# Kernel optimization log

Measured on AMD Instinct MI355X. Metric: run time of the kernel, lower is better.

Reference implementation:

```python
import jax, jax.numpy as jnp
import numpy as np

B, S, H = 2, 1024, 2048
HEADS = 16
QC = 1536      # q_compressed_dim
KVC = 512      # kv_compressed_dim
ROPE = 64      # qk_rope_dim
NOPE = H // HEADS  # 128, non-rope head dim
VH = 128       # v_head_dim
INTER = 1408   # MoE intermediate dim
NSH = 2        # shared experts
NRT = 8        # routed experts
TOPK = 2
EPS = 1e-6


def setup_inputs() -> dict:
    key = jax.random.key(0)
    ks = jax.random.split(key, 16)

    def w(k, shape, scale=0.02):
        return jax.random.normal(k, shape, jnp.float32) * scale

    return {
        "x": jax.random.normal(ks[0], (B, S, H), jnp.float32),
        "freq": jax.random.uniform(ks[1], (S, ROPE // 2), jnp.float32, 0.0, 2.0 * np.pi),
        "mask": jnp.zeros((S, S), jnp.float32),
        "w_attn_norm": jnp.ones((H,), jnp.float32),
        "w_ffn_norm": jnp.ones((H,), jnp.float32),
        "W_dq": w(ks[2], (H, QC)),
        "q_c_norm": jnp.ones((QC,), jnp.float32),
        "W_uq": w(ks[3], (QC, HEADS * (NOPE + ROPE))),
        "W_dkv": w(ks[4], (H, KVC + ROPE)),
        "kv_c_norm": jnp.ones((KVC,), jnp.float32),
        "W_ukv": w(ks[5], (KVC, HEADS * (NOPE + VH))),
        "W_o": w(ks[6], (HEADS * VH, H)),
        "W_r": w(ks[7], (H, NRT)),
        "Ws_gate": w(ks[8], (NSH, H, INTER)),
        "Ws_up": w(ks[9], (NSH, H, INTER)),
        "Ws_down": w(ks[10], (NSH, INTER, H)),
        "We_gate": w(ks[11], (NRT, H, INTER)),
        "We_up": w(ks[12], (NRT, H, INTER)),
        "We_down": w(ks[13], (NRT, INTER, H)),
    }


def rmsnorm(x, w):
    return x * jax.lax.rsqrt(jnp.mean(x * x, axis=-1, keepdims=True) + EPS) * w


def rope_apply(x, cos, sin):
    # x: [..., S, D]; cos/sin: [S, D/2], interleaved-pair rotation
    x1 = x[..., 0::2]
    x2 = x[..., 1::2]
    return jnp.stack([x1 * cos - x2 * sin, x1 * sin + x2 * cos], axis=-1).reshape(x.shape)


def _experts(t, Wg, Wu, Wd):
    # t: [T,H]; W*: [E,H,I]/[E,I,H] -> [E,T,H], SwiGLU per expert
    hid = jax.nn.silu(jnp.einsum('th,ehi->eti', t, Wg)) * jnp.einsum('th,ehi->eti', t, Wu)
    return jnp.einsum('eti,eih->eth', hid, Wd)


def reference(x, freq, mask, w_attn_norm, w_ffn_norm, W_dq, q_c_norm, W_uq, W_dkv,
              kv_c_norm, W_ukv, W_o, W_r, Ws_gate, Ws_up, Ws_down,
              We_gate, We_up, We_down):
    Bb, Ss, Hh = x.shape
    cos = jnp.cos(freq)
    sin = jnp.sin(freq)

    # ---- MLA attention (pre-norm) ----
    h = rmsnorm(x, w_attn_norm)
    cq = rmsnorm(h @ W_dq, q_c_norm)                              # [B,S,QC]
    q = (cq @ W_uq).reshape(Bb, Ss, HEADS, NOPE + ROPE).transpose(0, 2, 1, 3)
    q_nope, q_rope = q[..., :NOPE], q[..., NOPE:]
    q_rope = rope_apply(q_rope, cos, sin)                          # [B,Hh,S,ROPE]

    ckv = h @ W_dkv                                               # [B,S,KVC+ROPE]
    kv_c = rmsnorm(ckv[..., :KVC], kv_c_norm)
    k_rope = rope_apply(ckv[..., KVC:], cos, sin)                  # [B,S,ROPE] shared over heads
    kv = (kv_c @ W_ukv).reshape(Bb, Ss, HEADS, NOPE + VH).transpose(0, 2, 1, 3)
    k_nope, v = kv[..., :NOPE], kv[..., NOPE:]

    scale = 1.0 / np.sqrt(NOPE + ROPE)
    scores = (jnp.einsum('bhsd,bhtd->bhst', q_nope, k_nope)
              + jnp.einsum('bhsd,btd->bhst', q_rope, k_rope)) * scale + mask
    attn = jax.nn.softmax(scores, axis=-1)
    attn_out = jnp.einsum('bhst,bhtd->bshd', attn, v).reshape(Bb, Ss, HEADS * VH) @ W_o
    x = x + attn_out

    # ---- DeepSeekMoE FFN (pre-norm) ----
    t = rmsnorm(x, w_ffn_norm).reshape(Bb * Ss, Hh)
    shared = _experts(t, Ws_gate, Ws_up, Ws_down).sum(axis=0)      # [T,H]
    probs = jax.nn.softmax(t @ W_r, axis=-1)                       # [T,E]
    vals, idx = jax.lax.top_k(probs, TOPK)
    weights = (jax.nn.one_hot(idx, NRT, dtype=t.dtype) * vals[..., None]).sum(axis=1)  # [T,E]
    routed = jnp.einsum('eth,te->th', _experts(t, We_gate, We_up, We_down), weights)
    return x + (shared + routed).reshape(Bb, Ss, Hh)
```

## Files before the change

kernel.cpp:

```cpp
#include <hip/hip_runtime.h>

typedef __bf16 bf16;
typedef _Float16 f16;
typedef unsigned short u16;
typedef __bf16 bf16x8 __attribute__((ext_vector_type(8)));
typedef _Float16 f16x8 __attribute__((ext_vector_type(8)));
typedef unsigned short u16x8 __attribute__((ext_vector_type(8)));
typedef float f32x4 __attribute__((ext_vector_type(4)));

#define TOK   2048
#define SEQ   1024
#define HIDD  2048
#define NHEADS 16
#define QCD   1536
#define KVCD  512
#define ROPED 64
#define NOPED 128
#define QDIM  192
#define VHD   128
#define KVD   576
#define KVDP  640
#define INTERD 1408
#define GUD   2816
#define RMS_EPS 1e-6f
#define SPS   64.0f
#define OSC   (1.0f/4096.0f)

__device__ inline void split64(float v, f16& h, f16& l) {
    v *= SPS; h = (f16)v; l = (f16)(v - (float)h);
}

__device__ inline void gl_lds16(const void* g, void* l) {
    __builtin_amdgcn_global_load_lds(
        (const __attribute__((address_space(1))) void*)g,
        (__attribute__((address_space(3))) void*)l,
        16, 0, 0);
}

__global__ __launch_bounds__(256) void tconv_kernel(const float* __restrict__ src,
                                                    bf16* __restrict__ dst,
                                                    int K, int N, int Npad) {
    __shared__ float tile[32][33];
    int nb = blockIdx.x * 32, kb = blockIdx.y * 32;
    int tx = threadIdx.x & 31, ty = threadIdx.x >> 5;
#pragma unroll
    for (int i = 0; i < 32; i += 8) {
        int k = kb + ty + i, n = nb + tx;
        tile[ty + i][tx] = (k < K && n < N) ? src[(long)k * N + n] : 0.f;
    }
    __syncthreads();
#pragma unroll
    for (int i = 0; i < 32; i += 8) {
        int n = nb + ty + i, k = kb + tx;
        if (n < Npad && k < K) dst[(long)n * K + k] = (bf16)tile[tx][ty + i];
    }
}

__global__ __launch_bounds__(256) void tconv3h_kernel(const float* __restrict__ src,
                                                      f16* __restrict__ dst,
                                                      int K, int N, int Npad) {
    __shared__ float tile[32][33];
    int nb = blockIdx.x * 32, kb = blockIdx.y * 32;
    int tx = threadIdx.x & 31, ty = threadIdx.x >> 5;
#pragma unroll
    for (int i = 0; i < 32; i += 8) {
        int k = kb + ty + i, n = nb + tx;
        tile[ty + i][tx] = (k < K && n < N) ? src[(long)k * N + n] : 0.f;
    }
    __syncthreads();
#pragma unroll
    for (int i = 0; i < 32; i += 8) {
        int n = nb + ty + i, k = kb + tx;
        if (n < Npad && k < K) {
            f16 h, l; split64(tile[tx][ty + i], h, l);
            long base = (long)n * (3 * K) + k;
            dst[base] = h; dst[base + K] = l; dst[base + 2 * K] = h;
        }
    }
}

template<int F16, int TM, int TN>
__global__ __launch_bounds__(256) void gemm_bt_kernel(
    const u16* __restrict__ A, const u16* __restrict__ B, void* __restrict__ Cv,
    const float* __restrict__ aux, const int* __restrict__ idx,
    const int* __restrict__ cntPtr,
    int K, int lda, int ldb, int ldc,
    long sA, long sB, long sC,
    int mode, int auxLd, float osc)
{
    constexpr int AM = TM / 32;
    constexpr int AN = TN / 32;
    __shared__ u16 As[2][TM * 64];
    __shared__ u16 Bs[2][TN * 64];
    const int bn = blockIdx.x, bm = blockIdx.y, z = blockIdx.z;
    int cnt = 1 << 30;
    if (cntPtr) {
        cnt = *cntPtr;
        int pad = (cnt + TM - 1) & ~(TM - 1);
        if (bm * TM >= pad) return;
    }
    const int tid = threadIdx.x, lane = tid & 63, w = tid >> 6;
    const int wm = w >> 1, wn = w & 1;
    const int lr = lane & 15;
    const int srow = lane >> 3, c16 = lane & 7;
    const u16* Ab = A + (long)z * sA + (long)bm * TM * lda;
    const u16* Bb = B + (long)z * sB + (long)bn * TN * ldb;
    f32x4 acc[AM][AN] = {};

    auto stage = [&](int buf, int k0) {
#pragma unroll
        for (int i = 0; i < TM / 32; i++) {
            int rb = i * 32 + w * 8;
            int row = rb + srow;
            int gc = ((c16 ^ (row & 7)) << 3);
            gl_lds16(&Ab[(long)row * lda + k0 + gc], &As[buf][rb * 64]);
        }
#pragma unroll
        for (int i = 0; i < TN / 32; i++) {
            int rb = i * 32 + w * 8;
            int row = rb + srow;
            int gc = ((c16 ^ (row & 7)) << 3);
            gl_lds16(&Bb[(long)row * ldb + k0 + gc], &Bs[buf][rb * 64]);
        }
    };

    const int nk = K >> 6;
    stage(0, 0);
    __syncthreads();
    for (int t = 0; t < nk; ++t) {
        const int cur = t & 1;
        if (t + 1 < nk) stage(cur ^ 1, (t + 1) << 6);
#pragma unroll
        for (int ks = 0; ks < 2; ks++) {
            u16x8 af[AM], bfr[AN];
#pragma unroll
            for (int mi = 0; mi < AM; mi++) {
                int row = wm * (TM / 2) + mi * 16 + lr;
                int cg = (ks * 4 + (lane >> 4)) ^ (row & 7);
                af[mi] = *(const u16x8*)&As[cur][row * 64 + cg * 8];
            }
#pragma unroll
            for (int ni = 0; ni < AN; ni++) {
                int row = wn * (TN / 2) + ni * 16 + lr;
                int cg = (ks * 4 + (lane >> 4)) ^ (row & 7);
                bfr[ni] = *(const u16x8*)&Bs[cur][row * 64 + cg * 8];
            }
#pragma unroll
            for (int mi = 0; mi < AM; mi++)
#pragma unroll
                for (int ni = 0; ni < AN; ni++) {
                    if constexpr (F16)
                        acc[mi][ni] = __builtin_amdgcn_mfma_f32_16x16x32_f16(
                            __builtin_bit_cast(f16x8, af[mi]),
                            __builtin_bit_cast(f16x8, bfr[ni]), acc[mi][ni], 0, 0, 0);
                    else
                        acc[mi][ni] = __builtin_amdgcn_mfma_f32_16x16x32_bf16(
                            __builtin_bit_cast(bf16x8, af[mi]),
                            __builtin_bit_cast(bf16x8, bfr[ni]), acc[mi][ni], 0, 0, 0);
                }
        }
        __syncthreads();
    }

    const int r0 = (lane >> 4) << 2;
    const int rowBase = bm * TM + wm * (TM / 2);
    const int colBase = bn * TN + wn * (TN / 2);
#pragma unroll
    for (int mi = 0; mi < AM; mi++) {
#pragma unroll
        for (int ni = 0; ni < AN; ni++) {
#pragma unroll
            for (int r = 0; r < 4; r++) {
                int row = rowBase + mi * 16 + r0 + r;
                int col = colBase + ni * 16 + lr;
                float val = acc[mi][ni][r] * osc;
                long ci = (long)z * sC + (long)row * ldc + col;
                if (mode == 0) {
                    ((float*)Cv)[ci] = val;
                } else if (mode == 2) {
                    ((float*)Cv)[ci] = val + aux[(long)row * auxLd + col];
                } else if (mode == 3) {
                    float s = aux ? aux[(long)row * auxLd] : 1.f;
                    ((float*)Cv)[ci] += s * val;
                } else if (mode == 5) {
                    if (row < cnt) {
                        int tok = idx[row];
                        ((float*)Cv)[(long)tok * ldc + col] += aux[(long)tok * auxLd] * val;
                    }
                } else {
                    f16 h = (f16)val; f16 l = (f16)(val - (float)h);
                    ((f16*)Cv)[ci] = h; ((f16*)Cv)[ci + auxLd] = h; ((f16*)Cv)[ci + 2 * auxLd] = l;
                }
            }
        }
    }
}

__global__ __launch_bounds__(256) void rmsnorm_kernel(const float* __restrict__ in,
                                                      const float* __restrict__ w,
                                                      bf16* __restrict__ outB,
                                                      float* __restrict__ copyOut, int C) {
    long row = blockIdx.x;
    const float* r = in + row * C;
    float ss = 0.f;
    for (int i = threadIdx.x; i < C; i += 256) { float v = r[i]; ss += v * v; }
    for (int off = 32; off > 0; off >>= 1) ss += __shfl_down(ss, off, 64);
    __shared__ float red[5];
    int lane = threadIdx.x & 63, wv = threadIdx.x >> 6;
    if (lane == 0) red[wv] = ss;
    __syncthreads();
    if (threadIdx.x == 0) red[4] = rsqrtf((red[0] + red[1] + red[2] + red[3]) / C + RMS_EPS);
    __syncthreads();
    float sc = red[4];
    for (int i = threadIdx.x; i < C; i += 256) {
        outB[row * C + i] = (bf16)(r[i] * sc * w[i]);
        if (copyOut) copyOut[row * C + i] = r[i];
    }
}

__global__ __launch_bounds__(256) void rmsnorm3h_kernel(const float* __restrict__ in,
                                                        const float* __restrict__ w,
                                                        f16* __restrict__ out3, int C) {
    long row = blockIdx.x;
    const float* r = in + row * C;
    float ss = 0.f;
    for (int i = threadIdx.x; i < C; i += 256) { float v = r[i]; ss += v * v; }
    for (int off = 32; off > 0; off >>= 1) ss += __shfl_down(ss, off, 64);
    __shared__ float red[5];
    int lane = threadIdx.x & 63, wv = threadIdx.x >> 6;
    if (lane == 0) red[wv] = ss;
    __syncthreads();
    if (threadIdx.x == 0) red[4] = rsqrtf((red[0] + red[1] + red[2] + red[3]) / C + RMS_EPS);
    __syncthreads();
    float sc = red[4];
    f16* o = out3 + row * (3L * C);
    for (int i = threadIdx.x; i < C; i += 256) {
        f16 h, l; split64(r[i] * sc * w[i], h, l);
        o[i] = h; o[C + i] = h; o[2 * C + i] = l;
    }
}

__global__ __launch_bounds__(256) void kvsplit3h_kernel(const float* __restrict__ ckv,
                                                        const float* __restrict__ nrm,
                                                        const float* __restrict__ freq,
                                                        f16* __restrict__ kvc3,
                                                        float* __restrict__ krope) {
    int t = blockIdx.x; int s = t & (SEQ - 1);
    const float* r = ckv + (long)t * KVDP;
    float ss = 0.f;
    for (int i = threadIdx.x; i < KVCD; i += 256) { float v = r[i]; ss += v * v; }
    for (int off = 32; off > 0; off >>= 1) ss += __shfl_down(ss, off, 64);
    __shared__ float red[5];
    int lane = threadIdx.x & 63, wv = threadIdx.x >> 6;
    if (lane == 0) red[wv] = ss;
    __syncthreads();
    if (threadIdx.x == 0) red[4] = rsqrtf((red[0] + red[1] + red[2] + red[3]) / KVCD + RMS_EPS);
    __syncthreads();
    float sc = red[4];
    f16* o = kvc3 + (long)t * (3 * KVCD);
    for (int i = threadIdx.x; i < KVCD; i += 256) {
        f16 h, l; split64(r[i] * sc * nrm[i], h, l);
        o[i] = h; o[KVCD + i] = h; o[2 * KVCD + i] = l;
    }
    if (threadIdx.x < 32) {
        int i = threadIdx.x;
        float f = freq[s * 32 + i], c = cosf(f), sn = sinf(f);
        float x1 = r[KVCD + 2 * i], x2 = r[KVCD + 2 * i + 1];
        krope[(long)t * ROPED + 2 * i]     = x1 * c - x2 * sn;
        krope[(long)t * ROPED + 2 * i + 1] = x1 * sn + x2 * c;
    }
}

__global__ __launch_bounds__(256) void build_q3h_kernel(const float* __restrict__ qpre,
                                                        const float* __restrict__ freq,
                                                        f16* __restrict__ q3) {
    int t = blockIdx.x; int b = t >> 10, s = t & (SEQ - 1);
    for (int idx = threadIdx.x; idx < NHEADS * 96; idx += 256) {
        int h = idx / 96, j = idx % 96;
        const float* qrow = qpre + (long)t * 3072 + h * QDIM;
        f16* dst = q3 + ((long)(b * NHEADS + h) * SEQ + s) * (3 * QDIM);
        if (j < 64) {
            int d = 2 * j;
#pragma unroll
            for (int u = 0; u < 2; u++) {
                f16 hh, ll; split64(qrow[d + u], hh, ll);
                dst[d + u] = hh; dst[QDIM + d + u] = hh; dst[2 * QDIM + d + u] = ll;
            }
        } else {
            int i = j - 64;
            float f = freq[s * 32 + i], c = cosf(f), sn = sinf(f);
            float x1 = qrow[NOPED + 2 * i], x2 = qrow[NOPED + 2 * i + 1];
            float v0 = x1 * c - x2 * sn, v1 = x1 * sn + x2 * c;
            int d = NOPED + 2 * i;
            f16 h0, l0, h1, l1; split64(v0, h0, l0); split64(v1, h1, l1);
            dst[d] = h0; dst[QDIM + d] = h0; dst[2 * QDIM + d] = l0;
            dst[d + 1] = h1; dst[QDIM + d + 1] = h1; dst[2 * QDIM + d + 1] = l1;
        }
    }
}

__global__ __launch_bounds__(256) void build_k3h_kernel(const float* __restrict__ kv,
                                                        const float* __restrict__ krope,
                                                        f16* __restrict__ k3,
                                                        f16* __restrict__ v3T) {
    int t = blockIdx.x; int b = t >> 10, s = t & (SEQ - 1);
    const float* kvrow = kv + (long)t * 4096;
    const float* kr = krope + (long)t * ROPED;
    for (int idx = threadIdx.x; idx < NHEADS * 96; idx += 256) {
        int h = idx / 96, j = idx % 96;
        f16* dst = k3 + ((long)(b * NHEADS + h) * SEQ + s) * (3 * QDIM);
        float v0, v1; int d;
        if (j < 64) { d = 2 * j; v0 = kvrow[h * 256 + d]; v1 = kvrow[h * 256 + d + 1]; }
        else { int i = j - 64; d = NOPED + 2 * i; v0 = kr[2 * i]; v1 = kr[2 * i + 1]; }
        f16 h0, l0, h1, l1; split64(v0, h0, l0); split64(v1, h1, l1);
        dst[d] = h0; dst[QDIM + d] = l0; dst[2 * QDIM + d] = h0;
        dst[d + 1] = h1; dst[QDIM + d + 1] = l1; dst[2 * QDIM + d + 1] = h1;
    }
    for (int idx = threadIdx.x; idx < NHEADS * VHD; idx += 256) {
        int h = idx >> 7, d = idx & 127;
        f16 hh, ll; split64(kvrow[h * 256 + NOPED + d], hh, ll);
        long base = ((long)(b * NHEADS + h) * VHD + d) * (3 * SEQ) + s;
        v3T[base] = hh; v3T[base + SEQ] = ll; v3T[base + 2 * SEQ] = hh;
    }
}

__global__ __launch_bounds__(256) void softmax3h_kernel(const float* __restrict__ scores,
                                                        const float* __restrict__ mask,
                                                        f16* __restrict__ P3, float scale) {
    int s = blockIdx.x, h = blockIdx.y;
    const float* row  = scores + ((long)h * SEQ + s) * SEQ;
    const float* mrow = mask + (long)s * SEQ;
    f16* prow = P3 + ((long)h * SEQ + s) * (3 * SEQ);
    float v[4]; float m = -1e30f;
#pragma unroll
    for (int j = 0; j < 4; j++) {
        int i = threadIdx.x + j * 256;
        v[j] = row[i] * scale + mrow[i];
        m = fmaxf(m, v[j]);
    }
    for (int off = 32; off > 0; off >>= 1) m = fmaxf(m, __shfl_down(m, off, 64));
    __shared__ float redm[5], reds[5];
    int lane = threadIdx.x & 63, wv = threadIdx.x >> 6;
    if (lane == 0) redm[wv] = m;
    __syncthreads();
    if (threadIdx.x == 0) redm[4] = fmaxf(fmaxf(redm[0], redm[1]), fmaxf(redm[2], redm[3]));
    __syncthreads();
    float M = redm[4];
    float sum = 0.f;
#pragma unroll
    for (int j = 0; j < 4; j++) { v[j] = expf(v[j] - M); sum += v[j]; }
    for (int off = 32; off > 0; off >>= 1) sum += __shfl_down(sum, off, 64);
    if (lane == 0) reds[wv] = sum;
    __syncthreads();
    if (threadIdx.x == 0) reds[4] = reds[0] + reds[1] + reds[2] + reds[3];
    __syncthreads();
    float inv = 1.f / reds[4];
#pragma unroll
    for (int j = 0; j < 4; j++) {
        int i = threadIdx.x + j * 256;
        f16 hh, ll; split64(v[j] * inv, hh, ll);
        prow[i] = hh; prow[SEQ + i] = hh; prow[2 * SEQ + i] = ll;
    }
}

__global__ void zero_counts_kernel(int* counts) {
    if (threadIdx.x < 8) counts[threadIdx.x] = 0;
}

__global__ __launch_bounds__(64) void router_kernel(const float* __restrict__ x2,
                                                    const float* __restrict__ wffn,
                                                    const float* __restrict__ Wr,
                                                    float* __restrict__ wts,
                                                    int* __restrict__ perm,
                                                    int* __restrict__ counts) {
    int t = blockIdx.x; int lane = threadIdx.x;
    const float* r = x2 + (long)t * HIDD;
    float ss = 0.f;
    for (int k = lane; k < HIDD; k += 64) { float v = r[k]; ss += v * v; }
    for (int off = 32; off > 0; off >>= 1) ss += __shfl_down(ss, off, 64);
    float sc = rsqrtf(__shfl(ss, 0, 64) / HIDD + RMS_EPS);
    float acc[8] = {0, 0, 0, 0, 0, 0, 0, 0};
    for (int k = lane; k < HIDD; k += 64) {
        float tv = r[k] * sc * wffn[k];
        const float* wr = Wr + (long)k * 8;
#pragma unroll
        for (int e = 0; e < 8; e++) acc[e] += tv * wr[e];
    }
#pragma unroll
    for (int e = 0; e < 8; e++)
        for (int off = 32; off > 0; off >>= 1) acc[e] += __shfl_down(acc[e], off, 64);
    if (lane == 0) {
        float m = acc[0];
#pragma unroll
        for (int e = 1; e < 8; e++) m = fmaxf(m, acc[e]);
        float p[8]; float se = 0.f;
#pragma unroll
        for (int e = 0; e < 8; e++) { p[e] = expf(acc[e] - m); se += p[e]; }
        float inv = 1.f / se;
        int i1 = 0; float v1 = p[0];
        for (int e = 1; e < 8; e++) if (p[e] > v1) { v1 = p[e]; i1 = e; }
        int i2 = -1; float v2 = -1.f;
        for (int e = 0; e < 8; e++) if (e != i1 && p[e] > v2) { v2 = p[e]; i2 = e; }
#pragma unroll
        for (int e = 0; e < 8; e++)
            wts[(long)t * 8 + e] = (e == i1) ? v1 * inv : ((e == i2) ? v2 * inv : 0.f);
        int s1 = atomicAdd(&counts[i1], 1); perm[i1 * TOK + s1] = t;
        int s2 = atomicAdd(&counts[i2], 1); perm[i2 * TOK + s2] = t;
    }
}

__global__ __launch_bounds__(256) void gather_kernel(const bf16* __restrict__ tbuf,
                                                     const int* __restrict__ perm,
                                                     const int* __restrict__ cntPtr,
                                                     bf16* __restrict__ tA) {
    int row = blockIdx.x;
    int cnt = *cntPtr;
    int pad = (cnt + 127) & ~127;
    if (row >= pad) return;
    int i = threadIdx.x * 8;
    if (row < cnt) {
        int tok = perm[row];
        *(bf16x8*)&tA[(long)row * HIDD + i] = *(const bf16x8*)&tbuf[(long)tok * HIDD + i];
    } else {
        bf16x8 z = {};
        *(bf16x8*)&tA[(long)row * HIDD + i] = z;
    }
}

__global__ __launch_bounds__(256) void silumul_kernel(const float* __restrict__ gu,
                                                      bf16* __restrict__ hid,
                                                      const int* __restrict__ cntPtr) {
    long t = blockIdx.x;
    if (cntPtr) {
        int pad = (*cntPtr + 127) & ~127;
        if (t >= pad) return;
    }
    const float* row = gu + t * GUD;
    bf16* h = hid + t * INTERD;
    for (int i = threadIdx.x; i < INTERD; i += 256) {
        float g = row[i], u = row[INTERD + i];
        h[i] = (bf16)(g / (1.f + expf(-g)) * u);
    }
}

static inline size_t alignup(size_t v) { return (v + 255) & ~(size_t)255; }

extern "C" void kernel_launch(void* const* d_in, const int* in_sizes, int n_in,
                              void* d_out, int out_size, void* d_ws, size_t ws_size,
                              hipStream_t stream) {
    const float* x       = (const float*)d_in[0];
    const float* freq    = (const float*)d_in[1];
    const float* mask    = (const float*)d_in[2];
    const float* w_attn  = (const float*)d_in[3];
    const float* w_ffn   = (const float*)d_in[4];
    const float* W_dq    = (const float*)d_in[5];
    const float* q_c_nrm = (const float*)d_in[6];
    const float* W_uq    = (const float*)d_in[7];
    const float* W_dkv   = (const float*)d_in[8];
    const float* kv_nrm  = (const float*)d_in[9];
    const float* W_ukv   = (const float*)d_in[10];
    const float* W_o     = (const float*)d_in[11];
    const float* W_r     = (const float*)d_in[12];
    const float* Ws_gate = (const float*)d_in[13];
    const float* Ws_up   = (const float*)d_in[14];
    const float* Ws_down = (const float*)d_in[15];
    const float* We_gate = (const float*)d_in[16];
    const float* We_up   = (const float*)d_in[17];
    const float* We_down = (const float*)d_in[18];
    float* out = (float*)d_out;
    char* ws = (char*)d_ws;
    (void)in_sizes; (void)n_in; (void)out_size;

    size_t o = 0;
    auto alloc = [&](size_t n) { size_t r = o; o += alignup(n); return r; };
    size_t oWslot = alloc((size_t)3072 * 3 * QCD * 2);
    size_t oQ3    = alloc((size_t)32 * SEQ * 3 * QDIM * 2);
    size_t oK3    = alloc((size_t)32 * SEQ * 3 * QDIM * 2);
    size_t oV3T   = alloc((size_t)32 * VHD * 3 * SEQ * 2);
    size_t oAttn3 = alloc((size_t)TOK * 3 * HIDD * 2);
    size_t oX2    = alloc((size_t)TOK * HIDD * 4);
    size_t oTbuf  = alloc((size_t)TOK * HIDD * 2);
    size_t oTA    = alloc((size_t)TOK * HIDD * 2);
    size_t oWts   = alloc((size_t)TOK * 8 * 4);
    size_t oPerm  = alloc((size_t)8 * TOK * 4);
    size_t oCnt   = alloc((size_t)8 * 4);
    size_t oKrope = alloc((size_t)TOK * ROPED * 4);
    size_t zH3   = alignup((size_t)TOK * 3 * HIDD * 2);
    size_t zCqp  = alignup((size_t)TOK * QCD * 4);
    size_t zCq3  = alignup((size_t)TOK * 3 * QCD * 2);
    size_t zQp   = alignup((size_t)TOK * 3072 * 4);
    size_t zCkv  = alignup((size_t)TOK * KVDP * 4);
    size_t zKvc3 = alignup((size_t)TOK * 3 * KVCD * 2);
    size_t zKv   = alignup((size_t)TOK * 4096 * 4);
    size_t chain = zH3 + zCqp + zCq3 + zQp + zCkv + zKvc3 + zKv;
    size_t zScores = alignup((size_t)8 * SEQ * SEQ * 4);
    size_t zP3     = alignup((size_t)8 * SEQ * 3 * SEQ * 2);
    size_t zGu     = alignup((size_t)TOK * GUD * 4);
    size_t zHid    = alignup((size_t)TOK * INTERD * 2);
    size_t arenaSz = chain;
    if (zScores + zP3 > arenaSz) arenaSz = zScores + zP3;
    if (zGu + zHid > arenaSz) arenaSz = zGu + zHid;
    size_t oArena = alloc(arenaSz);
    if (ws_size < o) return;

    size_t oH3   = oArena;
    size_t oCqp  = oH3 + zH3;
    size_t oCq3  = oCqp + zCqp;
    size_t oQp   = oCq3 + zCq3;
    size_t oCkv  = oQp + zQp;
    size_t oKvc3 = oCkv + zCkv;
    size_t oKv   = oKvc3 + zKvc3;
    size_t oScores = oArena;
    size_t oP3     = oArena + zScores;
    size_t oGu     = oArena;
    size_t oHid    = oArena + zGu;

    f16*  wslotH = (f16*)(ws + oWslot);
    bf16* wslotB = (bf16*)(ws + oWslot);
    bf16* wslotB2 = (bf16*)(ws + oWslot + (size_t)GUD * HIDD * 2);
    f16*  q3    = (f16*)(ws + oQ3);
    f16*  k3    = (f16*)(ws + oK3);
    f16*  v3T   = (f16*)(ws + oV3T);
    f16*  attn3 = (f16*)(ws + oAttn3);
    float* x2   = (float*)(ws + oX2);
    bf16* tbuf  = (bf16*)(ws + oTbuf);
    bf16* tA    = (bf16*)(ws + oTA);
    float* wts  = (float*)(ws + oWts);
    int*  perm  = (int*)(ws + oPerm);
    int*  counts = (int*)(ws + oCnt);
    float* krope = (float*)(ws + oKrope);
    f16*  h3    = (f16*)(ws + oH3);
    float* cqpre = (float*)(ws + oCqp);
    f16*  cq3   = (f16*)(ws + oCq3);
    float* qpre = (float*)(ws + oQp);
    float* ckv  = (float*)(ws + oCkv);
    f16*  kvc3  = (f16*)(ws + oKvc3);
    float* kv   = (float*)(ws + oKv);
    float* scores = (float*)(ws + oScores);
    f16*  P3    = (f16*)(ws + oP3);
    float* gu   = (float*)(ws + oGu);
    bf16* hid   = (bf16*)(ws + oHid);

    auto tconv = [&](const float* src, bf16* dst, int K, int N, int Npad) {
        dim3 g((Npad + 31) / 32, (K + 31) / 32);
        tconv_kernel<<<g, 256, 0, stream>>>(src, dst, K, N, Npad);
    };
    auto tconv3h = [&](const float* src, f16* dst, int K, int N, int Npad) {
        dim3 g((Npad + 31) / 32, (K + 31) / 32);
        tconv3h_kernel<<<g, 256, 0, stream>>>(src, dst, K, N, Npad);
    };
    auto gH128x128 = [&](const f16* A, const f16* B, void* C, const float* aux,
                         int M, int N, int K, int lda, int ldb, int ldc,
                         long sA, long sB, long sC, int Z, int mode, int auxLd, float osc) {
        dim3 g(N / 128, M / 128, Z);
        gemm_bt_kernel<1, 128, 128><<<g, 256, 0, stream>>>((const u16*)A, (const u16*)B, C, aux,
            nullptr, nullptr, K, lda, ldb, ldc, sA, sB, sC, mode, auxLd, osc);
    };
    auto gH128x64 = [&](const f16* A, const f16* B, void* C, const float* aux,
                        int M, int N, int K, int lda, int ldb, int ldc,
                        long sA, long sB, long sC, int Z, int mode, int auxLd, float osc) {
        dim3 g(N / 64, M / 128, Z);
        gemm_bt_kernel<1, 128, 64><<<g, 256, 0, stream>>>((const u16*)A, (const u16*)B, C, aux,
            nullptr, nullptr, K, lda, ldb, ldc, sA, sB, sC, mode, auxLd, osc);
    };
    auto gH64x64 = [&](const f16* A, const f16* B, void* C, const float* aux,
                       int M, int N, int K, int lda, int ldb, int ldc,
                       long sA, long sB, long sC, int Z, int mode, int auxLd, float osc) {
        dim3 g(N / 64, M / 64, Z);
        gemm_bt_kernel<1, 64, 64><<<g, 256, 0, stream>>>((const u16*)A, (const u16*)B, C, aux,
            nullptr, nullptr, K, lda, ldb, ldc, sA, sB, sC, mode, auxLd, osc);
    };
    auto gB128x64 = [&](const bf16* A, const bf16* B, void* C,
                        const float* aux, const int* idx, const int* cnt,
                        int M, int N, int K, int lda, int ldb, int ldc, int mode, int auxLd) {
        dim3 g(N / 64, M / 128, 1);
        gemm_bt_kernel<0, 128, 64><<<g, 256, 0, stream>>>((const u16*)A, (const u16*)B, C, aux,
            idx, cnt, K, lda, ldb, ldc, 0, 0, 0, mode, auxLd, 1.0f);
    };
    auto gB64x64 = [&](const bf16* A, const bf16* B, void* C,
                       const float* aux, const int* idx, const int* cnt,
                       int M, int N, int K, int lda, int ldb, int ldc, int mode, int auxLd) {
        dim3 g(N / 64, M / 64, 1);
        gemm_bt_kernel<0, 64, 64><<<g, 256, 0, stream>>>((const u16*)A, (const u16*)B, C, aux,
            idx, cnt, K, lda, ldb, ldc, 0, 0, 0, mode, auxLd, 1.0f);
    };

    rmsnorm3h_kernel<<<TOK, 256, 0, stream>>>(x, w_attn, h3, HIDD);

    tconv3h(W_dq, wslotH, HIDD, QCD, QCD);
    gH128x64(h3, wslotH, cqpre, nullptr, TOK, QCD, 3 * HIDD, 3 * HIDD, 3 * HIDD, QCD,
             0, 0, 0, 1, 0, 0, OSC);
    rmsnorm3h_kernel<<<TOK, 256, 0, stream>>>(cqpre, q_c_nrm, cq3, QCD);

    tconv3h(W_uq, wslotH, QCD, 3072, 3072);
    gH128x64(cq3, wslotH, qpre, nullptr, TOK, 3072, 3 * QCD, 3 * QCD, 3 * QCD, 3072,
             0, 0, 0, 1, 0, 0, OSC);

    tconv3h(W_dkv, wslotH, HIDD, KVD, KVDP);
    gH64x64(h3, wslotH, ckv, nullptr, TOK, KVDP, 3 * HIDD, 3 * HIDD, 3 * HIDD, KVDP,
            0, 0, 0, 1, 0, 0, OSC);
    kvsplit3h_kernel<<<TOK, 256, 0, stream>>>(ckv, kv_nrm, freq, kvc3, krope);

    tconv3h(W_ukv, wslotH, KVCD, 4096, 4096);
    gH128x128(kvc3, wslotH, kv, nullptr, TOK, 4096, 3 * KVCD, 3 * KVCD, 3 * KVCD, 4096,
              0, 0, 0, 1, 0, 0, OSC);

    build_q3h_kernel<<<TOK, 256, 0, stream>>>(qpre, freq, q3);
    build_k3h_kernel<<<TOK, 256, 0, stream>>>(kv, krope, k3, v3T);

    const float scale = 1.f / sqrtf((float)QDIM);
    for (int b = 0; b < 2; b++) {
        for (int hc = 0; hc < 2; hc++) {
            int h0 = b * NHEADS + hc * 8;
            gH128x128(q3 + (size_t)h0 * SEQ * 3 * QDIM, k3 + (size_t)h0 * SEQ * 3 * QDIM,
                      scores, nullptr, SEQ, SEQ, 3 * QDIM, 3 * QDIM, 3 * QDIM, SEQ,
                      (long)SEQ * 3 * QDIM, (long)SEQ * 3 * QDIM, (long)SEQ * SEQ, 8, 0, 0, OSC);
            softmax3h_kernel<<<dim3(SEQ, 8), 256, 0, stream>>>(scores, mask, P3, scale);
            gH64x64(P3, v3T + (size_t)h0 * VHD * 3 * SEQ,
                    attn3 + (size_t)b * SEQ * 3 * HIDD + (size_t)(hc * 8) * VHD, nullptr,
                    SEQ, VHD, 3 * SEQ, 3 * SEQ, 3 * SEQ, 3 * HIDD,
                    (long)SEQ * 3 * SEQ, (long)VHD * 3 * SEQ, (long)VHD, 8, 6, HIDD,
                    1.0f / SPS);
        }
    }

    tconv3h(W_o, wslotH, HIDD, HIDD, HIDD);
    gH128x64(attn3, wslotH, x2, x, TOK, HIDD, 3 * HIDD, 3 * HIDD, 3 * HIDD, HIDD,
             0, 0, 0, 1, 2, HIDD, OSC);

    rmsnorm_kernel<<<TOK, 256, 0, stream>>>(x2, w_ffn, tbuf, out, HIDD);
    zero_counts_kernel<<<1, 64, 0, stream>>>(counts);
    router_kernel<<<TOK, 64, 0, stream>>>(x2, w_ffn, W_r, wts, perm, counts);

    for (int e = 0; e < 2; e++) {
        tconv(Ws_gate + (size_t)e * HIDD * INTERD, wslotB, HIDD, INTERD, INTERD);
        tconv(Ws_up   + (size_t)e * HIDD * INTERD, wslotB + (size_t)INTERD * HIDD, HIDD, INTERD, INTERD);
        gB128x64(tbuf, wslotB, gu, nullptr, nullptr, nullptr,
                 TOK, GUD, HIDD, HIDD, HIDD, GUD, 0, 0);
        silumul_kernel<<<TOK, 256, 0, stream>>>(gu, hid, nullptr);
        tconv(Ws_down + (size_t)e * INTERD * HIDD, wslotB2, INTERD, HIDD, HIDD);
        gB128x64(hid, wslotB2, out, nullptr, nullptr, nullptr,
                 TOK, HIDD, INTERD, INTERD, INTERD, HIDD, 3, 0);
    }
    for (int e = 0; e < 8; e++) {
        gather_kernel<<<TOK, 256, 0, stream>>>(tbuf, perm + (size_t)e * TOK, counts + e, tA);
        tconv(We_gate + (size_t)e * HIDD * INTERD, wslotB, HIDD, INTERD, INTERD);
        tconv(We_up   + (size_t)e * HIDD * INTERD, wslotB + (size_t)INTERD * HIDD, HIDD, INTERD, INTERD);
        gB64x64(tA, wslotB, gu, nullptr, nullptr, counts + e,
                TOK, GUD, HIDD, HIDD, HIDD, GUD, 0, 0);
        silumul_kernel<<<TOK, 256, 0, stream>>>(gu, hid, counts + e);
        tconv(We_down + (size_t)e * INTERD * HIDD, wslotB2, INTERD, HIDD, HIDD);
        gB64x64(hid, wslotB2, out, wts + e, perm + (size_t)e * TOK, counts + e,
                TOK, HIDD, INTERD, INTERD, INTERD, HIDD, 5, 8);
    }
}
```

Before: 1.728 ms.

## Remap GEMM blocks per XCD, batch all heads, fuse expert weight transposes

The GEMM kernel now remaps its linear block index so that each of the 8 XCDs gets a contiguous range of output tiles, which is meant to improve L2 locality across chiplets. The attention loop now launches the score GEMM, softmax and PV GEMM once per batch over all 16 heads instead of twice over 8 heads, and the scores and P buffers are doubled to fit. The three per-expert weight transpose/convert launches are merged into a single 3D-grid kernel. Together these cut launch count and try to raise occupancy, at the cost of a larger scratch arena and a remap that assumes round-robin dispatch across XCDs.

Result: slower. 1.814 ms (+5.0%).

```diff
diff --git a/kernel.cpp b/kernel.cpp
--- a/kernel.cpp
+++ b/kernel.cpp
@@ -56,6 +56,28 @@
     }
 }
 
+__global__ __launch_bounds__(256) void tconv_ex3_kernel(const float* __restrict__ gate,
+                                                        const float* __restrict__ up,
+                                                        const float* __restrict__ down,
+                                                        bf16* __restrict__ dGU,
+                                                        bf16* __restrict__ dD) {
+    const float* src; bf16* dst; int K, N;
+    if (blockIdx.z == 0)      { src = gate; dst = dGU;                          K = HIDD;   N = INTERD; }
+    else if (blockIdx.z == 1) { src = up;   dst = dGU + (size_t)INTERD * HIDD;  K = HIDD;   N = INTERD; }
+    else                      { src = down; dst = dD;                           K = INTERD; N = HIDD; }
+    int nb = blockIdx.x * 32, kb = blockIdx.y * 32;
+    if (nb >= N || kb >= K) return;
+    __shared__ float tile[32][33];
+    int tx = threadIdx.x & 31, ty = threadIdx.x >> 5;
+#pragma unroll
+    for (int i = 0; i < 32; i += 8)
+        tile[ty + i][tx] = src[(long)(kb + ty + i) * N + nb + tx];
+    __syncthreads();
+#pragma unroll
+    for (int i = 0; i < 32; i += 8)
+        dst[(long)(nb + ty + i) * K + kb + tx] = (bf16)tile[tx][ty + i];
+}
+
 __global__ __launch_bounds__(256) void tconv3h_kernel(const float* __restrict__ src,
                                                       f16* __restrict__ dst,
                                                       int K, int N, int Npad) {
@@ -92,7 +114,18 @@
     constexpr int AN = TN / 32;
     __shared__ u16 As[2][TM * 64];
     __shared__ u16 Bs[2][TN * 64];
-    const int bn = blockIdx.x, bm = blockIdx.y, z = blockIdx.z;
+    int bn, bm;
+    {
+        int gx = gridDim.x;
+        int total = gx * gridDim.y;
+        int lin = blockIdx.y * gx + blockIdx.x;
+        int q8 = total >> 3, r8 = total & 7;
+        int xcd = lin & 7, pos = lin >> 3;
+        int nl = (xcd < r8) ? xcd * (q8 + 1) + pos
+                            : r8 * (q8 + 1) + (xcd - r8) * q8 + pos;
+        bm = nl / gx; bn = nl - bm * gx;
+    }
+    const int z = blockIdx.z;
     int cnt = 1 << 30;
     if (cntPtr) {
         cnt = *cntPtr;
@@ -493,8 +526,8 @@
     size_t zKvc3 = alignup((size_t)TOK * 3 * KVCD * 2);
     size_t zKv   = alignup((size_t)TOK * 4096 * 4);
     size_t chain = zH3 + zCqp + zCq3 + zQp + zCkv + zKvc3 + zKv;
-    size_t zScores = alignup((size_t)8 * SEQ * SEQ * 4);
-    size_t zP3     = alignup((size_t)8 * SEQ * 3 * SEQ * 2);
+    size_t zScores = alignup((size_t)16 * SEQ * SEQ * 4);
+    size_t zP3     = alignup((size_t)16 * SEQ * 3 * SEQ * 2);
     size_t zGu     = alignup((size_t)TOK * GUD * 4);
     size_t zHid    = alignup((size_t)TOK * INTERD * 2);
     size_t arenaSz = chain;
@@ -541,13 +574,12 @@
     float* gu   = (float*)(ws + oGu);
     bf16* hid   = (bf16*)(ws + oHid);
 
-    auto tconv = [&](const float* src, bf16* dst, int K, int N, int Npad) {
-        dim3 g((Npad + 31) / 32, (K + 31) / 32);
-        tconv_kernel<<<g, 256, 0, stream>>>(src, dst, K, N, Npad);
-    };
     auto tconv3h = [&](const float* src, f16* dst, int K, int N, int Npad) {
         dim3 g((Npad + 31) / 32, (K + 31) / 32);
         tconv3h_kernel<<<g, 256, 0, stream>>>(src, dst, K, N, Npad);
+    };
+    auto tconvEx = [&](const float* gate, const float* up, const float* down) {
+        tconv_ex3_kernel<<<dim3(64, 64, 3), 256, 0, stream>>>(gate, up, down, wslotB, wslotB2);
     };
     auto gH128x128 = [&](const f16* A, const f16* B, void* C, const float* aux,
                          int M, int N, int K, int lda, int ldb, int ldc,
@@ -608,20 +640,18 @@
     build_q3h_kernel<<<TOK, 256, 0, stream>>>(qpre, freq, q3);
     build_k3h_kernel<<<TOK, 256, 0, stream>>>(kv, krope, k3, v3T);
 
-    const float scale = 1.f / sqrtf((float)QDIM);
     for (int b = 0; b < 2; b++) {
-        for (int hc = 0; hc < 2; hc++) {
-            int h0 = b * NHEADS + hc * 8;
-            gH128x128(q3 + (size_t)h0 * SEQ * 3 * QDIM, k3 + (size_t)h0 * SEQ * 3 * QDIM,
-                      scores, nullptr, SEQ, SEQ, 3 * QDIM, 3 * QDIM, 3 * QDIM, SEQ,
-                      (long)SEQ * 3 * QDIM, (long)SEQ * 3 * QDIM, (long)SEQ * SEQ, 8, 0, 0, OSC);
-            softmax3h_kernel<<<dim3(SEQ, 8), 256, 0, stream>>>(scores, mask, P3, scale);
-            gH64x64(P3, v3T + (size_t)h0 * VHD * 3 * SEQ,
-                    attn3 + (size_t)b * SEQ * 3 * HIDD + (size_t)(hc * 8) * VHD, nullptr,
-                    SEQ, VHD, 3 * SEQ, 3 * SEQ, 3 * SEQ, 3 * HIDD,
-                    (long)SEQ * 3 * SEQ, (long)VHD * 3 * SEQ, (long)VHD, 8, 6, HIDD,
-                    1.0f / SPS);
-        }
+        int h0 = b * NHEADS;
+        gH128x128(q3 + (size_t)h0 * SEQ * 3 * QDIM, k3 + (size_t)h0 * SEQ * 3 * QDIM,
+                  scores, nullptr, SEQ, SEQ, 3 * QDIM, 3 * QDIM, 3 * QDIM, SEQ,
+                  (long)SEQ * 3 * QDIM, (long)SEQ * 3 * QDIM, (long)SEQ * SEQ, 16, 0, 0, OSC);
+        softmax3h_kernel<<<dim3(SEQ, 16), 256, 0, stream>>>(scores, mask, P3,
+                                                            1.f / sqrtf((float)QDIM));
+        gH64x64(P3, v3T + (size_t)h0 * VHD * 3 * SEQ,
+                attn3 + (size_t)b * SEQ * 3 * HIDD, nullptr,
+                SEQ, VHD, 3 * SEQ, 3 * SEQ, 3 * SEQ, 3 * HIDD,
+                (long)SEQ * 3 * SEQ, (long)VHD * 3 * SEQ, (long)VHD, 16, 6, HIDD,
+                1.0f / SPS);
     }
 
     tconv3h(W_o, wslotH, HIDD, HIDD, HIDD);
@@ -633,23 +663,23 @@
     router_kernel<<<TOK, 64, 0, stream>>>(x2, w_ffn, W_r, wts, perm, counts);
 
     for (int e = 0; e < 2; e++) {
-        tconv(Ws_gate + (size_t)e * HIDD * INTERD, wslotB, HIDD, INTERD, INTERD);
-        tconv(Ws_up   + (size_t)e * HIDD * INTERD, wslotB + (size_t)INTERD * HIDD, HIDD, INTERD, INTERD);
+        tconvEx(Ws_gate + (size_t)e * HIDD * INTERD,
+                Ws_up   + (size_t)e * HIDD * INTERD,
+                Ws_down + (size_t)e * INTERD * HIDD);
         gB128x64(tbuf, wslotB, gu, nullptr, nullptr, nullptr,
                  TOK, GUD, HIDD, HIDD, HIDD, GUD, 0, 0);
         silumul_kernel<<<TOK, 256, 0, stream>>>(gu, hid, nullptr);
-        tconv(Ws_down + (size_t)e * INTERD * HIDD, wslotB2, INTERD, HIDD, HIDD);
         gB128x64(hid, wslotB2, out, nullptr, nullptr, nullptr,
                  TOK, HIDD, INTERD, INTERD, INTERD, HIDD, 3, 0);
     }
     for (int e = 0; e < 8; e++) {
         gather_kernel<<<TOK, 256, 0, stream>>>(tbuf, perm + (size_t)e * TOK, counts + e, tA);
-        tconv(We_gate + (size_t)e * HIDD * INTERD, wslotB, HIDD, INTERD, INTERD);
-        tconv(We_up   + (size_t)e * HIDD * INTERD, wslotB + (size_t)INTERD * HIDD, HIDD, INTERD, INTERD);
+        tconvEx(We_gate + (size_t)e * HIDD * INTERD,
+                We_up   + (size_t)e * HIDD * INTERD,
+                We_down + (size_t)e * INTERD * HIDD);
         gB64x64(tA, wslotB, gu, nullptr, nullptr, counts + e,
                 TOK, GUD, HIDD, HIDD, HIDD, GUD, 0, 0);
         silumul_kernel<<<TOK, 256, 0, stream>>>(gu, hid, counts + e);
-        tconv(We_down + (size_t)e * INTERD * HIDD, wslotB2, INTERD, HIDD, HIDD);
         gB64x64(hid, wslotB2, out, wts + e, perm + (size_t)e * TOK, counts + e,
                 TOK, HIDD, INTERD, INTERD, INTERD, HIDD, 5, 8);
     }
```
